# Optimization experiments

Hardware: AMD Instinct MI355X
Metric: run time of the kernel (lower is better)

## Reference

```python
import jax, jax.numpy as jnp
import numpy as np

B = 64          # graphs per batch
N = 131072      # total nodes (B * 2048)
E = 524288      # total edges
V = 32000       # embedding vocab
D_IN = 256      # embed.output_size
D = 128         # GCN hidden size


def setup_inputs() -> dict:
    key = jax.random.key(0)
    ks = jax.random.split(key, 9)
    return {
        "node_tokens": jax.random.randint(ks[0], (N,), 0, V),
        "edge_index": jax.random.randint(ks[1], (2, E), 0, N),
        "embed_table": jax.random.normal(ks[2], (V, D_IN), jnp.float32),
        "W_node_w": jax.random.normal(ks[3], (D, D_IN), jnp.float32) * 0.02,
        "W_node_b": jax.random.normal(ks[4], (D,), jnp.float32) * 0.02,
        "conv1_w": jax.random.normal(ks[5], (D, D), jnp.float32) * 0.02,
        "conv1_b": jax.random.normal(ks[6], (D,), jnp.float32) * 0.02,
        "conv2_w": jax.random.normal(ks[7], (D, D), jnp.float32) * 0.02,
        "conv2_b": jax.random.normal(ks[8], (D,), jnp.float32) * 0.02,
    }


def _gcn_conv(x, src, dst, norm, W, b):
    # PyG GCNConv: linear first, then normalized scatter-add aggregation, then bias.
    x = x @ W.T                                        # [N, D]
    msg = x[src] * norm[:, None]                       # gather + per-edge scale
    out = jax.ops.segment_sum(msg, dst, num_segments=N)  # scatter-add at dst
    return out + b


def reference(node_tokens, edge_index, embed_table, W_node_w, W_node_b,
              conv1_w, conv1_b, conv2_w, conv2_b):
    # compute_node_features: embed lookup -> W_node linear (no mask path)
    x = embed_table[node_tokens] @ W_node_w.T + W_node_b   # [N, D]

    # GCNConv normalization with self-loops (shared by both layers)
    loop = jnp.arange(N)
    src = jnp.concatenate([edge_index[0], loop])
    dst = jnp.concatenate([edge_index[1], loop])
    deg = jax.ops.segment_sum(jnp.ones(E + N, x.dtype), dst, num_segments=N)
    dinv = jnp.where(deg > 0, jax.lax.rsqrt(deg), 0.0)
    norm = dinv[src] * dinv[dst]                           # [E+N]

    x = jax.nn.relu(_gcn_conv(x, src, dst, norm, conv1_w, conv1_b))
    x = _gcn_conv(x, src, dst, norm, conv2_w, conv2_b)

    # Unpad into [B, max_n, D]; equal-length graphs, no edge tokens -> reshape.
    n = N // B
    output = x.reshape(B, n, D)          # dropout_p=0 -> identity
    labels = node_tokens.reshape(B, n)
    labels_mask = jnp.ones((B, n), dtype=bool)
    label_node_ids = jnp.broadcast_to(jnp.arange(n), (B, n))
    return output, labels, labels_mask, label_node_ids
```

## Files before the change

kernel.cpp:

```cpp
#include <hip/hip_runtime.h>
#include <hip/hip_bf16.h>

#define N_NODES 131072
#define N_EDGES 524288
#define DHID    128
#define DIN     256
#define VOCAB   32000

typedef __attribute__((ext_vector_type(8))) short short8;
typedef __attribute__((ext_vector_type(4))) float floatx4;

__device__ inline short bf16_rne(float f) {
    union { float f; unsigned u; } v; v.f = f;
    unsigned r = v.u + 0x7FFF + ((v.u >> 16) & 1);
    return (short)(r >> 16);
}
__device__ inline float bf16_to_f(short s) {
    union { unsigned u; float f; } v; v.u = ((unsigned)(unsigned short)s) << 16;
    return v.f;
}
__device__ inline short8 cvt8(float4 lo, float4 hi) {
    short8 o;
    o[0] = bf16_rne(lo.x); o[1] = bf16_rne(lo.y);
    o[2] = bf16_rne(lo.z); o[3] = bf16_rne(lo.w);
    o[4] = bf16_rne(hi.x); o[5] = bf16_rne(hi.y);
    o[6] = bf16_rne(hi.z); o[7] = bf16_rne(hi.w);
    return o;
}


#define MEGA_VB 250
#define MEGA_WB 128
#define MEGA_TOTAL (MEGA_VB + MEGA_WB + N_EDGES / 256)

__global__ __launch_bounds__(256) void mega(const float* __restrict__ emb,
                                            const float* __restrict__ Wn,
                                            short* __restrict__ z,
                                            const float* __restrict__ W1,
                                            const float* __restrict__ W2,
                                            short* __restrict__ W1b,
                                            short* __restrict__ W2b,
                                            const int* __restrict__ edst,
                                            int* __restrict__ counts) {
    const int b = blockIdx.x;
    if (b < MEGA_VB) {
        const int t = threadIdx.x;
        const int wid  = t >> 6;
        const int lane = t & 63;
        const int col  = lane & 15;
        const int quad = lane >> 4;
        const int vbase = b * 128 + wid * 32;
        const size_t row0 = (size_t)(vbase + col);
        const size_t row1 = (size_t)(vbase + 16 + col);

        floatx4 acc[2][8] = {};
#pragma unroll
        for (int kc = 0; kc < DIN / 32; ++kc) {
            const int ko = kc * 32 + quad * 8;
            short8 a0 = cvt8(*(const float4*)&emb[row0 * DIN + ko],
                             *(const float4*)&emb[row0 * DIN + ko + 4]);
            short8 a1 = cvt8(*(const float4*)&emb[row1 * DIN + ko],
                             *(const float4*)&emb[row1 * DIN + ko + 4]);
#pragma unroll
            for (int ft = 0; ft < 8; ++ft) {
                const size_t wr = (size_t)(col * 8 + ft) * DIN + ko;
                short8 bb = cvt8(*(const float4*)&Wn[wr],
                                 *(const float4*)&Wn[wr + 4]);
                acc[0][ft] = __builtin_amdgcn_mfma_f32_16x16x32_bf16(a0, bb, acc[0][ft], 0, 0, 0);
                acc[1][ft] = __builtin_amdgcn_mfma_f32_16x16x32_bf16(a1, bb, acc[1][ft], 0, 0, 0);
            }
        }
#pragma unroll
        for (int mt = 0; mt < 2; ++mt) {
#pragma unroll
            for (int r = 0; r < 4; ++r) {
                const int row = vbase + mt * 16 + quad * 4 + r;
                short8 o;
#pragma unroll
                for (int ft = 0; ft < 8; ++ft)
                    o[ft] = bf16_rne(acc[mt][ft][r]);
                *(short8*)&z[(size_t)row * DHID + col * 8] = o;
            }
        }
    } else if (b < MEGA_VB + MEGA_WB) {
        int i = (b - MEGA_VB) * 256 + threadIdx.x;
        if (i < 16384) W1b[i] = bf16_rne(W1[i]);
        else           W2b[i - 16384] = bf16_rne(W2[i - 16384]);
    } else {
        int e = (b - MEGA_VB - MEGA_WB) * 256 + threadIdx.x;
        atomicAdd(&counts[edst[e]], 1);
    }
}


__global__ __launch_bounds__(256) void alloc_csr(const int* __restrict__ counts,
                                                 int* __restrict__ offsets,
                                                 int* __restrict__ cursor,
                                                 float* __restrict__ dinv,
                                                 int* __restrict__ total,
                                                 const int* __restrict__ tok,
                                                 float* __restrict__ meta_out) {
    __shared__ int s[256];
    __shared__ int base;
    int i = blockIdx.x * 256 + threadIdx.x;
    int v = counts[i];
    s[threadIdx.x] = v;
    __syncthreads();
    for (int d = 1; d < 256; d <<= 1) {
        int t = (threadIdx.x >= d) ? s[threadIdx.x - d] : 0;
        __syncthreads();
        s[threadIdx.x] += t;
        __syncthreads();
    }
    int incl = s[threadIdx.x];
    if (threadIdx.x == 255) base = atomicAdd(total, incl);
    __syncthreads();
    int off = base + incl - v;
    offsets[i] = off;
    cursor[i]  = off;
    dinv[i] = rsqrtf((float)(v + 1));

    const size_t L0 = (size_t)N_NODES * DHID;
    __builtin_nontemporal_store((float)tok[i],     &meta_out[L0 + i]);
    __builtin_nontemporal_store(1.0f,              &meta_out[L0 + N_NODES + i]);
    __builtin_nontemporal_store((float)(i & 2047), &meta_out[L0 + 2 * N_NODES + i]);
}


__global__ __launch_bounds__(256) void fill_csr(const int* __restrict__ src,
                                                const int* __restrict__ dst,
                                                int* __restrict__ cursor,
                                                const int* __restrict__ counts,
                                                const int* __restrict__ tok,
                                                int* __restrict__ csr1,
                                                int* __restrict__ csr2) {
    int e = blockIdx.x * 256 + threadIdx.x;
    int d = dst[e];
    int s = src[e];
    int p = atomicAdd(&cursor[d], 1);
    int deg = counts[s];
    csr1[p] = (deg << 24) | tok[s];
    csr2[p] = (deg << 24) | s;
}


template <bool RELU, bool OUT_BF16, bool ZG>
__global__ __launch_bounds__(256, 8) void fused_conv(const short* __restrict__ x,
                                                     const int* __restrict__ csr,
                                                     const int* __restrict__ offsets,
                                                     const int* __restrict__ counts,
                                                     const float* __restrict__ dinv,
                                                     const int* __restrict__ tok,
                                                     const float* __restrict__ bn,
                                                     const short* __restrict__ Wb,
                                                     const float* __restrict__ bias,
                                                     void* __restrict__ outp) {
    const int t = threadIdx.x;
    const int wid  = t >> 6;
    const int lane = t & 63;
    const int col  = lane & 15;
    const int quad = lane >> 4;
    const int base = (blockIdx.x * 4 + wid) * 16;
    const int node = base + col;

    const float di = dinv[node];
    const int beg = offsets[node];
    const int cnt = counts[node];
    const int* pcsr = csr + beg;

    float af[4][8];
    {
        const int self = ZG ? tok[node] : node;
        const size_t xrow = (size_t)self * DHID + quad * 8;
#pragma unroll
        for (int c = 0; c < 4; ++c) {
            short8 v = *(const short8*)&x[xrow + c * 32];
#pragma unroll
            for (int j = 0; j < 8; ++j) af[c][j] = di * bf16_to_f(v[j]);
        }
    }
    float sw = di;

    int cn = (cnt > 0) ? pcsr[0] : 0;
    for (int e = 0; e < cnt; ++e) {
        const int   s = cn & 0xFFFFFF;
        const float w = rsqrtf((float)(((unsigned)cn >> 24) + 1));
        if (e + 1 < cnt) cn = pcsr[e + 1];
        if (ZG) sw += w;
        const size_t r0 = (size_t)s * DHID + quad * 8;
        short8 u0 = *(const short8*)&x[r0];
        short8 u1 = *(const short8*)&x[r0 + 32];
        short8 u2 = *(const short8*)&x[r0 + 64];
        short8 u3 = *(const short8*)&x[r0 + 96];
#pragma unroll
        for (int j = 0; j < 8; ++j) {
            af[0][j] = fmaf(w, bf16_to_f(u0[j]), af[0][j]);
            af[1][j] = fmaf(w, bf16_to_f(u1[j]), af[1][j]);
            af[2][j] = fmaf(w, bf16_to_f(u2[j]), af[2][j]);
            af[3][j] = fmaf(w, bf16_to_f(u3[j]), af[3][j]);
        }
    }

    short8 a[4];
#pragma unroll
    for (int c = 0; c < 4; ++c) {
        if (ZG) {
            const float4 b0 = *(const float4*)&bn[c * 32 + quad * 8];
            const float4 b1 = *(const float4*)&bn[c * 32 + quad * 8 + 4];
            const float bv[8] = {b0.x, b0.y, b0.z, b0.w, b1.x, b1.y, b1.z, b1.w};
#pragma unroll
            for (int j = 0; j < 8; ++j)
                a[c][j] = bf16_rne(di * (af[c][j] + sw * bv[j]));
        } else {
#pragma unroll
            for (int j = 0; j < 8; ++j) a[c][j] = bf16_rne(di * af[c][j]);
        }
    }

    floatx4 acc[8] = {};
#pragma unroll
    for (int c = 0; c < 4; ++c) {
        const int ko = c * 32 + quad * 8;
#pragma unroll
        for (int ft = 0; ft < 8; ++ft) {
            short8 b = *(const short8*)&Wb[(size_t)(col * 8 + ft) * DHID + ko];
            acc[ft] = __builtin_amdgcn_mfma_f32_16x16x32_bf16(a[c], b, acc[ft], 0, 0, 0);
        }
    }

    const float4 bv0 = *(const float4*)&bias[col * 8];
    const float4 bv1 = *(const float4*)&bias[col * 8 + 4];
    const float bb[8] = {bv0.x, bv0.y, bv0.z, bv0.w, bv1.x, bv1.y, bv1.z, bv1.w};
    short* outb = (short*)outp;
    float* outf = (float*)outp;
#pragma unroll
    for (int r = 0; r < 4; ++r) {
        const size_t row = (size_t)(base + quad * 4 + r) * DHID + col * 8;
        if (OUT_BF16) {
            short8 o;
#pragma unroll
            for (int ft = 0; ft < 8; ++ft) {
                float v = acc[ft][r] + bb[ft];
                if (RELU) v = fmaxf(v, 0.f);
                o[ft] = bf16_rne(v);
            }
            *(short8*)&outb[row] = o;
        } else {
            floatx4 o0, o1;
            o0[0] = acc[0][r] + bb[0]; o0[1] = acc[1][r] + bb[1];
            o0[2] = acc[2][r] + bb[2]; o0[3] = acc[3][r] + bb[3];
            o1[0] = acc[4][r] + bb[4]; o1[1] = acc[5][r] + bb[5];
            o1[2] = acc[6][r] + bb[6]; o1[3] = acc[7][r] + bb[7];
            if (RELU) {
#pragma unroll
                for (int k = 0; k < 4; ++k) {
                    o0[k] = fmaxf(o0[k], 0.f);
                    o1[k] = fmaxf(o1[k], 0.f);
                }
            }
            __builtin_nontemporal_store(o0, (floatx4*)&outf[row]);
            __builtin_nontemporal_store(o1, (floatx4*)&outf[row + 4]);
        }
    }
}


extern "C" void kernel_launch(void* const* d_in, const int* in_sizes, int n_in,
                              void* d_out, int out_size, void* d_ws, size_t ws_size,
                              hipStream_t stream) {
    const int*   tok  = (const int*)d_in[0];
    const int*   esrc = (const int*)d_in[1];
    const int*   edst = esrc + N_EDGES;
    const float* emb  = (const float*)d_in[2];
    const float* Wn   = (const float*)d_in[3];
    const float* bn   = (const float*)d_in[4];
    const float* W1   = (const float*)d_in[5];
    const float* b1   = (const float*)d_in[6];
    const float* W2   = (const float*)d_in[7];
    const float* b2   = (const float*)d_in[8];
    float* out = (float*)d_out;

    char* ws = (char*)d_ws;
    int*   counts  = (int*)(ws);
    int*   total   = (int*)(ws + (1u << 19));
    int*   offsets = (int*)(ws + (1u << 19) + 256);
    int*   cursor  = (int*)(ws + (2u << 19) + 256);
    float* dinv    = (float*)(ws + (3u << 19) + 256);
    int*   csr1    = (int*)(ws + 3 * (1u << 20));
    int*   csr2    = (int*)(ws + 5 * (1u << 20));
    short* W1b     = (short*)(ws + 7 * (1u << 20));
    short* W2b     = (short*)(ws + 7 * (1u << 20) + (1u << 15));
    short* z       = (short*)(ws + 8 * (1u << 20));
    short* x2b     = (short*)(ws + 16 * (1u << 20));

    hipMemsetAsync(counts, 0, (1u << 19) + 256, stream);
    mega<<<MEGA_TOTAL, 256, 0, stream>>>(emb, Wn, z, W1, W2, W1b, W2b, edst, counts);
    alloc_csr<<<N_NODES / 256, 256, 0, stream>>>(counts, offsets, cursor, dinv,
                                                 total, tok, out);
    fill_csr<<<N_EDGES / 256, 256, 0, stream>>>(esrc, edst, cursor, counts, tok,
                                                csr1, csr2);

    fused_conv<true, true, true><<<N_NODES / 64, 256, 0, stream>>>(
        z, csr1, offsets, counts, dinv, tok, bn, W1b, b1, x2b);
    fused_conv<false, false, false><<<N_NODES / 64, 256, 0, stream>>>(
        x2b, csr2, offsets, counts, dinv, tok, bn, W2b, b2, out);
}
```

Before: 294.5 us.

## Move embedding GEMM into CSR fill kernel and interleave CSR arrays

Splits the edge-counting atomics into a small standalone kernel that reads four destinations per thread with an int4 load. The vocab GEMM and weight conversion now run in the same launch as the CSR fill, so the GEMM overlaps the scatter instead of the counting pass. The two CSR arrays are packed into one int2 array so a single scattered write stores both entries. Each conv pass now reads 8-byte entries and uses only half of each, which doubles its neighbor-list traffic.

```diff
diff --git a/kernel.cpp b/kernel.cpp
--- a/kernel.cpp
+++ b/kernel.cpp
@@ -29,67 +29,14 @@
 }
 
 
-#define MEGA_VB 250
-#define MEGA_WB 128
-#define MEGA_TOTAL (MEGA_VB + MEGA_WB + N_EDGES / 256)
-
-__global__ __launch_bounds__(256) void mega(const float* __restrict__ emb,
-                                            const float* __restrict__ Wn,
-                                            short* __restrict__ z,
-                                            const float* __restrict__ W1,
-                                            const float* __restrict__ W2,
-                                            short* __restrict__ W1b,
-                                            short* __restrict__ W2b,
-                                            const int* __restrict__ edst,
-                                            int* __restrict__ counts) {
-    const int b = blockIdx.x;
-    if (b < MEGA_VB) {
-        const int t = threadIdx.x;
-        const int wid  = t >> 6;
-        const int lane = t & 63;
-        const int col  = lane & 15;
-        const int quad = lane >> 4;
-        const int vbase = b * 128 + wid * 32;
-        const size_t row0 = (size_t)(vbase + col);
-        const size_t row1 = (size_t)(vbase + 16 + col);
-
-        floatx4 acc[2][8] = {};
-#pragma unroll
-        for (int kc = 0; kc < DIN / 32; ++kc) {
-            const int ko = kc * 32 + quad * 8;
-            short8 a0 = cvt8(*(const float4*)&emb[row0 * DIN + ko],
-                             *(const float4*)&emb[row0 * DIN + ko + 4]);
-            short8 a1 = cvt8(*(const float4*)&emb[row1 * DIN + ko],
-                             *(const float4*)&emb[row1 * DIN + ko + 4]);
-#pragma unroll
-            for (int ft = 0; ft < 8; ++ft) {
-                const size_t wr = (size_t)(col * 8 + ft) * DIN + ko;
-                short8 bb = cvt8(*(const float4*)&Wn[wr],
-                                 *(const float4*)&Wn[wr + 4]);
-                acc[0][ft] = __builtin_amdgcn_mfma_f32_16x16x32_bf16(a0, bb, acc[0][ft], 0, 0, 0);
-                acc[1][ft] = __builtin_amdgcn_mfma_f32_16x16x32_bf16(a1, bb, acc[1][ft], 0, 0, 0);
-            }
-        }
-#pragma unroll
-        for (int mt = 0; mt < 2; ++mt) {
-#pragma unroll
-            for (int r = 0; r < 4; ++r) {
-                const int row = vbase + mt * 16 + quad * 4 + r;
-                short8 o;
-#pragma unroll
-                for (int ft = 0; ft < 8; ++ft)
-                    o[ft] = bf16_rne(acc[mt][ft][r]);
-                *(short8*)&z[(size_t)row * DHID + col * 8] = o;
-            }
-        }
-    } else if (b < MEGA_VB + MEGA_WB) {
-        int i = (b - MEGA_VB) * 256 + threadIdx.x;
-        if (i < 16384) W1b[i] = bf16_rne(W1[i]);
-        else           W2b[i - 16384] = bf16_rne(W2[i - 16384]);
-    } else {
-        int e = (b - MEGA_VB - MEGA_WB) * 256 + threadIdx.x;
-        atomicAdd(&counts[edst[e]], 1);
-    }
+__global__ __launch_bounds__(256) void count_edges(const int* __restrict__ edst,
+                                                   int* __restrict__ counts) {
+    int i = blockIdx.x * 256 + threadIdx.x;
+    int4 e = ((const int4*)edst)[i];
+    atomicAdd(&counts[e.x], 1);
+    atomicAdd(&counts[e.y], 1);
+    atomicAdd(&counts[e.z], 1);
+    atomicAdd(&counts[e.w], 1);
 }
 
 
@@ -127,26 +74,83 @@
 }
 
 
-__global__ __launch_bounds__(256) void fill_csr(const int* __restrict__ src,
-                                                const int* __restrict__ dst,
-                                                int* __restrict__ cursor,
-                                                const int* __restrict__ counts,
-                                                const int* __restrict__ tok,
-                                                int* __restrict__ csr1,
-                                                int* __restrict__ csr2) {
-    int e = blockIdx.x * 256 + threadIdx.x;
-    int d = dst[e];
-    int s = src[e];
-    int p = atomicAdd(&cursor[d], 1);
-    int deg = counts[s];
-    csr1[p] = (deg << 24) | tok[s];
-    csr2[p] = (deg << 24) | s;
+#define FG_GEMM  250
+#define FG_WCONV 128
+#define FG_FILL  (N_EDGES / 256)
+#define FG_TOTAL (FG_GEMM + FG_WCONV + FG_FILL)
+
+__global__ __launch_bounds__(256) void fill_gemm(const float* __restrict__ emb,
+                                                 const float* __restrict__ Wn,
+                                                 short* __restrict__ z,
+                                                 const float* __restrict__ W1,
+                                                 const float* __restrict__ W2,
+                                                 short* __restrict__ W1b,
+                                                 short* __restrict__ W2b,
+                                                 const int* __restrict__ src,
+                                                 const int* __restrict__ dst,
+                                                 int* __restrict__ cursor,
+                                                 const int* __restrict__ counts,
+                                                 const int* __restrict__ tok,
+                                                 int2* __restrict__ csr) {
+    const int b = blockIdx.x;
+    if (b < FG_GEMM) {
+        const int t = threadIdx.x;
+        const int wid  = t >> 6;
+        const int lane = t & 63;
+        const int col  = lane & 15;
+        const int quad = lane >> 4;
+        const int vbase = b * 128 + wid * 32;
+        const size_t row0 = (size_t)(vbase + col);
+        const size_t row1 = (size_t)(vbase + 16 + col);
+
+        floatx4 acc[2][8] = {};
+#pragma unroll
+        for (int kc = 0; kc < DIN / 32; ++kc) {
+            const int ko = kc * 32 + quad * 8;
+            short8 a0 = cvt8(*(const float4*)&emb[row0 * DIN + ko],
+                             *(const float4*)&emb[row0 * DIN + ko + 4]);
+            short8 a1 = cvt8(*(const float4*)&emb[row1 * DIN + ko],
+                             *(const float4*)&emb[row1 * DIN + ko + 4]);
+#pragma unroll
+            for (int ft = 0; ft < 8; ++ft) {
+                const size_t wr = (size_t)(col * 8 + ft) * DIN + ko;
+                short8 bb = cvt8(*(const float4*)&Wn[wr],
+                                 *(const float4*)&Wn[wr + 4]);
+                acc[0][ft] = __builtin_amdgcn_mfma_f32_16x16x32_bf16(a0, bb, acc[0][ft], 0, 0, 0);
+                acc[1][ft] = __builtin_amdgcn_mfma_f32_16x16x32_bf16(a1, bb, acc[1][ft], 0, 0, 0);
+            }
+        }
+#pragma unroll
+        for (int mt = 0; mt < 2; ++mt) {
+#pragma unroll
+            for (int r = 0; r < 4; ++r) {
+                const int row = vbase + mt * 16 + quad * 4 + r;
+                short8 o;
+#pragma unroll
+                for (int ft = 0; ft < 8; ++ft)
+                    o[ft] = bf16_rne(acc[mt][ft][r]);
+                *(short8*)&z[(size_t)row * DHID + col * 8] = o;
+            }
+        }
+    } else if (b < FG_GEMM + FG_WCONV) {
+        int i = (b - FG_GEMM) * 256 + threadIdx.x;
+        if (i < 16384) W1b[i] = bf16_rne(W1[i]);
+        else           W2b[i - 16384] = bf16_rne(W2[i - 16384]);
+    } else {
+        int e = (b - FG_GEMM - FG_WCONV) * 256 + threadIdx.x;
+        int d = dst[e];
+        int s = src[e];
+        int p = atomicAdd(&cursor[d], 1);
+        int deg = counts[s];
+        csr[p] = make_int2((deg << 24) | tok[s],
+                           (deg << 24) | s);
+    }
 }
 
 
 template <bool RELU, bool OUT_BF16, bool ZG>
 __global__ __launch_bounds__(256, 8) void fused_conv(const short* __restrict__ x,
-                                                     const int* __restrict__ csr,
+                                                     const int2* __restrict__ csr,
                                                      const int* __restrict__ offsets,
                                                      const int* __restrict__ counts,
                                                      const float* __restrict__ dinv,
@@ -166,7 +170,7 @@
     const float di = dinv[node];
     const int beg = offsets[node];
     const int cnt = counts[node];
-    const int* pcsr = csr + beg;
+    const int2* pcsr = csr + beg;
 
     float af[4][8];
     {
@@ -181,10 +185,11 @@
     }
     float sw = di;
 
-    int cn = (cnt > 0) ? pcsr[0] : 0;
+    int2 cn = (cnt > 0) ? pcsr[0] : make_int2(0, 0);
     for (int e = 0; e < cnt; ++e) {
-        const int   s = cn & 0xFFFFFF;
-        const float w = rsqrtf((float)(((unsigned)cn >> 24) + 1));
+        const int   ce = ZG ? cn.x : cn.y;
+        const int   s  = ce & 0xFFFFFF;
+        const float w  = rsqrtf((float)(((unsigned)ce >> 24) + 1));
         if (e + 1 < cnt) cn = pcsr[e + 1];
         if (ZG) sw += w;
         const size_t r0 = (size_t)s * DHID + quad * 8;
@@ -286,22 +291,21 @@
     int*   offsets = (int*)(ws + (1u << 19) + 256);
     int*   cursor  = (int*)(ws + (2u << 19) + 256);
     float* dinv    = (float*)(ws + (3u << 19) + 256);
-    int*   csr1    = (int*)(ws + 3 * (1u << 20));
-    int*   csr2    = (int*)(ws + 5 * (1u << 20));
+    int2*  csr     = (int2*)(ws + 3 * (1u << 20));
     short* W1b     = (short*)(ws + 7 * (1u << 20));
     short* W2b     = (short*)(ws + 7 * (1u << 20) + (1u << 15));
     short* z       = (short*)(ws + 8 * (1u << 20));
     short* x2b     = (short*)(ws + 16 * (1u << 20));
 
     hipMemsetAsync(counts, 0, (1u << 19) + 256, stream);
-    mega<<<MEGA_TOTAL, 256, 0, stream>>>(emb, Wn, z, W1, W2, W1b, W2b, edst, counts);
+    count_edges<<<N_EDGES / 1024, 256, 0, stream>>>(edst, counts);
     alloc_csr<<<N_NODES / 256, 256, 0, stream>>>(counts, offsets, cursor, dinv,
                                                  total, tok, out);
-    fill_csr<<<N_EDGES / 256, 256, 0, stream>>>(esrc, edst, cursor, counts, tok,
-                                                csr1, csr2);
+    fill_gemm<<<FG_TOTAL, 256, 0, stream>>>(emb, Wn, z, W1, W2, W1b, W2b,
+                                            esrc, edst, cursor, counts, tok, csr);
 
     fused_conv<true, true, true><<<N_NODES / 64, 256, 0, stream>>>(
-        z, csr1, offsets, counts, dinv, tok, bn, W1b, b1, x2b);
+        z, csr, offsets, counts, dinv, tok, bn, W1b, b1, x2b);
     fused_conv<false, false, false><<<N_NODES / 64, 256, 0, stream>>>(
-        x2b, csr2, offsets, counts, dinv, tok, bn, W2b, b2, out);
-}
+        x2b, csr, offsets, counts, dinv, tok, bn, W2b, b2, out);
+}
```

Result: no change. 296.2 us (+0.6%).
